# Optimization experiments

Hardware: AMD Instinct MI355X
Metric: run time of the kernel (lower is better)

The kernel has to match this reference:

```python
import jax, jax.numpy as jnp
import numpy as np

N_NODES = 100000
N_EDGES = 3200000


def _norm_weights(edge_index, n):
    # Append self loops (GCNConv gcn_norm adds them back after the module's A - I)
    loops = jnp.arange(n, dtype=edge_index.dtype)
    row = jnp.concatenate([edge_index[0], loops])
    col = jnp.concatenate([edge_index[1], loops])
    ones = jnp.ones(row.shape[0], dtype=jnp.float32)
    deg = jax.ops.segment_sum(ones, row, num_segments=n)
    dinv = jnp.where(deg > 0, jax.lax.rsqrt(deg), 0.0)
    w = dinv[row] * dinv[col]  # symmetric normalization D^-1/2 (A+I) D^-1/2
    return row, col, w


def _spmm(row, col, w, h, n):
    # out[i] = sum_{(i,j) in E} w_ij * h[j]
    return jax.ops.segment_sum(w[:, None] * h[col], row, num_segments=n)


def setup_inputs() -> dict:
    key = jax.random.key(0)
    ks = jax.random.split(key, 4)
    x = jax.random.normal(ks[0], (N_NODES, 512), dtype=jnp.float32)
    W1 = jax.random.normal(ks[1], (512, 16), dtype=jnp.float32) * (1.0 / np.sqrt(512))
    b1 = jnp.zeros((16,), dtype=jnp.float32)
    W2 = jax.random.normal(ks[2], (16, 40), dtype=jnp.float32) * (1.0 / np.sqrt(16))
    b2 = jnp.zeros((40,), dtype=jnp.float32)
    edge_index = jax.random.randint(ks[3], (2, N_EDGES), 0, N_NODES, dtype=jnp.int64)
    return {"x": x, "W1": W1, "b1": b1, "W2": W2, "b2": b2, "edge_index": edge_index}


def reference(x, W1, b1, W2, b2, edge_index):
    n = x.shape[0]
    row, col, w = _norm_weights(edge_index, n)
    # GCNConv layer 1: A_norm @ (x W1) + b1, then relu (dropout is identity in eval)
    h = _spmm(row, col, w, x @ W1, n) + b1
    h = jax.nn.relu(h)
    # GCNConv layer 2 (same adjacency: adj2 is a clone of adj1)
    out = _spmm(row, col, w, h @ W2, n) + b2
    return jax.nn.log_softmax(out, axis=1)
```

## Files before the change

### kernel.cpp

```cpp
#include <hip/hip_runtime.h>
#include <hip/hip_fp16.h>
#include <math.h>

#define F0 512
#define F1 16
#define F2 40
#define CB_SHIFT 8
#define CB_ROWS 256
#define NCB_MAX 512
#define CAPCB 9216
#define EPB 8192
#define COL_BITS 17
#define CMASK ((1 << COL_BITS) - 1)
#define CNT_STRIDE 16

__global__ void k_zero(int* p, int m) {
    int i = blockIdx.x * blockDim.x + threadIdx.x;
    if (i < m) p[i] = 0;
}

__global__ __launch_bounds__(512) void k_fill(const int* __restrict__ row,
                                              const int* __restrict__ col, int E,
                                              int* cnt, int* __restrict__ ebuf,
                                              int NCB) {
    __shared__ int hcnt[NCB_MAX];
    __shared__ int lexcl[NCB_MAX];
    __shared__ int hbase[NCB_MAX];
    __shared__ int part[NCB_MAX];
    __shared__ int sorted[EPB];
    int t = threadIdx.x;
    int e0 = blockIdx.x * EPB;
    int nloc = min(EPB, E - e0);
    if (t < NCB_MAX) hcnt[t] = 0;
    __syncthreads();

    int rr[16], cc[16];
#pragma unroll
    for (int k = 0; k < 4; k++) {
        int base = t * 4 + k * 2048;
        if (base + 3 < nloc) {
            int4 r4 = *(const int4*)(row + e0 + base);
            int4 c4 = *(const int4*)(col + e0 + base);
            rr[k * 4 + 0] = r4.x; rr[k * 4 + 1] = r4.y;
            rr[k * 4 + 2] = r4.z; rr[k * 4 + 3] = r4.w;
            cc[k * 4 + 0] = c4.x; cc[k * 4 + 1] = c4.y;
            cc[k * 4 + 2] = c4.z; cc[k * 4 + 3] = c4.w;
        } else {
#pragma unroll
            for (int q = 0; q < 4; q++) {
                int e = base + q;
                rr[k * 4 + q] = (e < nloc) ? row[e0 + e] : -1;
                cc[k * 4 + q] = (e < nloc) ? col[e0 + e] : 0;
            }
        }
    }
#pragma unroll
    for (int q = 0; q < 16; q++)
        if (rr[q] >= 0) atomicAdd(&hcnt[rr[q] >> CB_SHIFT], 1);
    __syncthreads();
    int myv = hcnt[t];
    part[t] = myv;
    __syncthreads();
    for (int off = 1; off < NCB_MAX; off <<= 1) {
        int a = (t >= off) ? part[t - off] : 0;
        __syncthreads();
        part[t] += a;
        __syncthreads();
    }
    lexcl[t] = part[t] - myv;
    hbase[t] = (myv > 0) ? atomicAdd(&cnt[t * CNT_STRIDE], myv) : 0;
    hcnt[t] = 0;
    __syncthreads();
#pragma unroll
    for (int q = 0; q < 16; q++) {
        int r = rr[q];
        if (r >= 0) {
            int cb = r >> CB_SHIFT;
            int p = lexcl[cb] + atomicAdd(&hcnt[cb], 1);
            sorted[p] = ((r & (CB_ROWS - 1)) << COL_BITS) | cc[q];
        }
    }
    __syncthreads();
    int wv = t >> 6, lane = t & 63;
    for (int cb = wv; cb < NCB; cb += 8) {
        int c = hcnt[cb];
        int ls = lexcl[cb];
        int* dst = ebuf + (size_t)cb * CAPCB + hbase[cb];
        for (int j = lane; j < c; j += 64) dst[j] = sorted[ls + j];
    }
}

__global__ __launch_bounds__(512) void k_scan2(const int* __restrict__ cnt, int NCB,
                                               int* __restrict__ sbbase) {
    __shared__ int part[NCB_MAX];
    int t = threadIdx.x;
    int v = (t < NCB) ? cnt[t * CNT_STRIDE] : 0;
    part[t] = v;
    __syncthreads();
    for (int off = 1; off < NCB_MAX; off <<= 1) {
        int a = (t >= off) ? part[t - off] : 0;
        __syncthreads();
        part[t] += a;
        __syncthreads();
    }
    if (t < NCB) sbbase[t] = part[t] - v;
}

__global__ __launch_bounds__(256) void k_sort(const int* __restrict__ cnt,
                                              const int* __restrict__ sbbase,
                                              const int* __restrict__ ebuf, int n,
                                              int* __restrict__ colsort,
                                              int* __restrict__ deg,
                                              int* __restrict__ rs,
                                              float* __restrict__ dinv) {
    __shared__ int rcnt[CB_ROWS];
    __shared__ int rexcl[CB_ROWS];
    __shared__ int sorted[CAPCB];
    int cb = blockIdx.x;
    int t = threadIdx.x;
    int c = cnt[cb * CNT_STRIDE];
    const int* seg = ebuf + (size_t)cb * CAPCB;
    rcnt[t] = 0;
    __syncthreads();
    for (int base = t * 4; base < c; base += 1024) {
        if (base + 3 < c) {
            int4 v = *(const int4*)(seg + base);
            atomicAdd(&rcnt[v.x >> COL_BITS], 1);
            atomicAdd(&rcnt[v.y >> COL_BITS], 1);
            atomicAdd(&rcnt[v.z >> COL_BITS], 1);
            atomicAdd(&rcnt[v.w >> COL_BITS], 1);
        } else {
            for (int k = base; k < c; k++) atomicAdd(&rcnt[seg[k] >> COL_BITS], 1);
        }
    }
    __syncthreads();
    int myc = rcnt[t];
    rexcl[t] = myc;
    __syncthreads();
    for (int off = 1; off < CB_ROWS; off <<= 1) {
        int a = (t >= off) ? rexcl[t - off] : 0;
        __syncthreads();
        rexcl[t] += a;
        __syncthreads();
    }
    int excl = rexcl[t] - myc;
    int gbase = sbbase[cb];
    int i = (cb << CB_SHIFT) + t;
    if (i < n) {
        deg[i] = myc;
        rs[i] = gbase + excl;
        dinv[i] = rsqrtf((float)(myc + 1));
    }
    rcnt[t] = excl;
    __syncthreads();
    for (int base = t * 4; base < c; base += 1024) {
        if (base + 3 < c) {
            int4 v = *(const int4*)(seg + base);
            int p0 = atomicAdd(&rcnt[v.x >> COL_BITS], 1); sorted[p0] = v.x & CMASK;
            int p1 = atomicAdd(&rcnt[v.y >> COL_BITS], 1); sorted[p1] = v.y & CMASK;
            int p2 = atomicAdd(&rcnt[v.z >> COL_BITS], 1); sorted[p2] = v.z & CMASK;
            int p3 = atomicAdd(&rcnt[v.w >> COL_BITS], 1); sorted[p3] = v.w & CMASK;
        } else {
            for (int k = base; k < c; k++) {
                int v = seg[k];
                int p = atomicAdd(&rcnt[v >> COL_BITS], 1);
                sorted[p] = v & CMASK;
            }
        }
    }
    __syncthreads();
    for (int j = t; j < c; j += 256) colsort[gbase + j] = sorted[j];
}

__global__ __launch_bounds__(256, 2) void k_gemm1(const float* __restrict__ x,
                                                  const float* __restrict__ W1,
                                                  const float* __restrict__ dinv,
                                                  __half* __restrict__ hp, int n,
                                                  int total_waves) {
    int lane = threadIdx.x & 63;
    int wid = blockIdx.x * (blockDim.x >> 6) + (threadIdx.x >> 6);

    float w[8][16];
#pragma unroll
    for (int h = 0; h < 2; h++) {
#pragma unroll
        for (int r = 0; r < 4; r++) {
            int k = h * 256 + 4 * lane + r;
            const float4* p = (const float4*)(W1 + k * 16);
            float4 a = p[0], b = p[1], c = p[2], d = p[3];
            float* wr = w[h * 4 + r];
            wr[0] = a.x; wr[1] = a.y; wr[2] = a.z; wr[3] = a.w;
            wr[4] = b.x; wr[5] = b.y; wr[6] = b.z; wr[7] = b.w;
            wr[8] = c.x; wr[9] = c.y; wr[10] = c.z; wr[11] = c.w;
            wr[12] = d.x; wr[13] = d.y; wr[14] = d.z; wr[15] = d.w;
        }
    }

    for (int i0 = wid * 4; i0 < n; i0 += total_waves * 4) {
        float4 xq[8];
        if (i0 + 3 < n) {
            const float4* xp = (const float4*)(x + (size_t)i0 * F0);
#pragma unroll
            for (int q = 0; q < 8; q++) xq[q] = xp[q * 64 + lane];
        } else {
#pragma unroll
            for (int q = 0; q < 8; q++) {
                int r = q >> 1;
                if (i0 + r < n) {
                    const float4* xp = (const float4*)(x + (size_t)(i0 + r) * F0);
                    xq[q] = xp[(q & 1) * 64 + lane];
                } else {
                    xq[q] = make_float4(0.f, 0.f, 0.f, 0.f);
                }
            }
        }
        bool b0 = (lane & 1) != 0;
        bool b1 = (lane & 2) != 0;
        bool b2 = (lane & 4) != 0;
        bool b3 = (lane & 8) != 0;
#pragma unroll
        for (int r = 0; r < 4; r++) {
            float4 xa = xq[2 * r], xb = xq[2 * r + 1];
            float v16[16];
#pragma unroll
            for (int j = 0; j < 16; j++) {
                v16[j] = xa.x * w[0][j] + xa.y * w[1][j] + xa.z * w[2][j] + xa.w * w[3][j]
                       + xb.x * w[4][j] + xb.y * w[5][j] + xb.z * w[6][j] + xb.w * w[7][j];
            }
            float v8[8];
#pragma unroll
            for (int t2 = 0; t2 < 8; t2++) {
                float a = v16[2 * t2], b = v16[2 * t2 + 1];
                float keep = b0 ? b : a;
                float send = b0 ? a : b;
                v8[t2] = keep + __shfl_xor(send, 1);
            }
            float v4[4];
#pragma unroll
            for (int t2 = 0; t2 < 4; t2++) {
                float a = v8[2 * t2], b = v8[2 * t2 + 1];
                float keep = b1 ? b : a;
                float send = b1 ? a : b;
                v4[t2] = keep + __shfl_xor(send, 2);
            }
            float v2[2];
#pragma unroll
            for (int t2 = 0; t2 < 2; t2++) {
                float a = v4[2 * t2], b = v4[2 * t2 + 1];
                float keep = b2 ? b : a;
                float send = b2 ? a : b;
                v2[t2] = keep + __shfl_xor(send, 4);
            }
            float keep = b3 ? v2[1] : v2[0];
            float send = b3 ? v2[0] : v2[1];
            float v1 = keep + __shfl_xor(send, 8);
            v1 += __shfl_xor(v1, 16);
            v1 += __shfl_xor(v1, 32);
            int i = i0 + r;
            if (lane < 16 && i < n)
                hp[(size_t)i * F1 + lane] = __float2half_rn(dinv[i] * v1);
        }
    }
}

__global__ __launch_bounds__(256) void k_spmm1(const __half* __restrict__ hp,
                                               const int* __restrict__ rs,
                                               const int* __restrict__ deg,
                                               const int* __restrict__ colsort,
                                               const float* __restrict__ dinv,
                                               const float* __restrict__ b1,
                                               __half* __restrict__ s2, int n) {
    int t = threadIdx.x;
    int lane = t & 63;
    int g = lane >> 4;
    int jf = lane & 15;
    int i = blockIdx.x * 4 + (t >> 6);
    if (i >= n) return;
    int s = rs[i], c = deg[i];
    float acc = (g == 0) ? __half2float(hp[(size_t)i * F1 + jf]) : 0.f;
    int e = g;
    for (; e + 12 < c; e += 16) {
        int c0 = colsort[s + e];
        int c1 = colsort[s + e + 4];
        int c2 = colsort[s + e + 8];
        int c3 = colsort[s + e + 12];
        float v0 = __half2float(hp[(size_t)c0 * F1 + jf]);
        float v1 = __half2float(hp[(size_t)c1 * F1 + jf]);
        float v2 = __half2float(hp[(size_t)c2 * F1 + jf]);
        float v3 = __half2float(hp[(size_t)c3 * F1 + jf]);
        acc += (v0 + v1) + (v2 + v3);
    }
    for (; e < c; e += 4)
        acc += __half2float(hp[(size_t)colsort[s + e] * F1 + jf]);
    acc += __shfl_xor(acc, 16);
    acc += __shfl_xor(acc, 32);
    float di = dinv[i];
    float h1 = fmaxf(di * acc + b1[jf], 0.f);
    if (lane < 16) s2[(size_t)i * F1 + jf] = __float2half_rn(di * h1);
}

__global__ __launch_bounds__(256) void k_spmm2(const __half* __restrict__ s2,
                                               const int* __restrict__ rs,
                                               const int* __restrict__ deg,
                                               const int* __restrict__ colsort,
                                               const float* __restrict__ dinv,
                                               const float* __restrict__ W2,
                                               const float* __restrict__ b2,
                                               float* __restrict__ out, int n) {
    __shared__ float sW2[F1 * F2];
    int t = threadIdx.x;
    for (int idx = t; idx < F1 * F2; idx += 256) sW2[idx] = W2[idx];
    __syncthreads();

    int lane = t & 63;
    int g = lane >> 4;
    int jf = lane & 15;
    int i = blockIdx.x * 4 + (t >> 6);
    if (i >= n) return;
    int s = rs[i], c = deg[i];
    float acc = (g == 0) ? __half2float(s2[(size_t)i * F1 + jf]) : 0.f;
    int e = g;
    for (; e + 12 < c; e += 16) {
        int c0 = colsort[s + e];
        int c1 = colsort[s + e + 4];
        int c2 = colsort[s + e + 8];
        int c3 = colsort[s + e + 12];
        float v0 = __half2float(s2[(size_t)c0 * F1 + jf]);
        float v1 = __half2float(s2[(size_t)c1 * F1 + jf]);
        float v2 = __half2float(s2[(size_t)c2 * F1 + jf]);
        float v3 = __half2float(s2[(size_t)c3 * F1 + jf]);
        acc += (v0 + v1) + (v2 + v3);
    }
    for (; e < c; e += 4)
        acc += __half2float(s2[(size_t)colsort[s + e] * F1 + jf]);
    acc += __shfl_xor(acc, 16);
    acc += __shfl_xor(acc, 32);
    float z = dinv[i] * acc;

    bool act = lane < F2;
    int k = act ? lane : 0;
    float o = 0.f;
#pragma unroll
    for (int j = 0; j < F1; j++) {
        float zj = __shfl(z, j);
        o += zj * sW2[j * F2 + k];
    }
    float val = act ? o + b2[k] : -INFINITY;
    float m = val;
#pragma unroll
    for (int off = 1; off < 64; off <<= 1) m = fmaxf(m, __shfl_xor(m, off));
    float ex = act ? __expf(val - m) : 0.f;
    float ssum = ex;
#pragma unroll
    for (int off = 1; off < 64; off <<= 1) ssum += __shfl_xor(ssum, off);
    if (act) out[(size_t)i * F2 + lane] = val - m - __logf(ssum);
}

extern "C" void kernel_launch(void* const* d_in, const int* in_sizes, int n_in,
                              void* d_out, int out_size, void* d_ws, size_t ws_size,
                              hipStream_t stream) {
    const float* x  = (const float*)d_in[0];
    const float* W1 = (const float*)d_in[1];
    const float* b1 = (const float*)d_in[2];
    const float* W2 = (const float*)d_in[3];
    const float* b2 = (const float*)d_in[4];
    const int*   ei = (const int*)d_in[5];

    int n = in_sizes[0] / F0;
    int E = in_sizes[5] / 2;
    const int* row = ei;
    const int* col = ei + E;
    int NCB = (n + CB_ROWS - 1) >> CB_SHIFT;

    int* deg     = (int*)d_ws;
    int* rs      = deg + n;
    float* dinv  = (float*)(rs + n);
    int* cnt     = (int*)(dinv + n);
    int* sbbase  = cnt + NCB_MAX * CNT_STRIDE;
    int* colsort = sbbase + NCB_MAX;
    int* ebuf    = colsort + E;
    __half* hp   = (__half*)ebuf;
    __half* s2   = hp + (size_t)n * F1;

    int nchunks = (E + EPB - 1) / EPB;
    k_zero<<<(NCB * CNT_STRIDE + 255) / 256, 256, 0, stream>>>(cnt, NCB * CNT_STRIDE);
    k_fill<<<nchunks, 512, 0, stream>>>(row, col, E, cnt, ebuf, NCB);
    k_scan2<<<1, NCB_MAX, 0, stream>>>(cnt, NCB, sbbase);
    k_sort<<<NCB, 256, 0, stream>>>(cnt, sbbase, ebuf, n, colsort, deg, rs, dinv);

    int g1_blocks = 2048;
    k_gemm1<<<g1_blocks, 256, 0, stream>>>(x, W1, dinv, hp, n, g1_blocks * 4);
    k_spmm1<<<(n + 3) / 4, 256, 0, stream>>>(hp, rs, deg, colsort, dinv, b1, s2, n);
    k_spmm2<<<(n + 3) / 4, 256, 0, stream>>>(s2, rs, deg, colsort, dinv, W2, b2,
                                             (float*)d_out, n);
}
```

Measured before the change: 478.4 us.

## Map one node per 16 lanes in SpMM kernels instead of one per wavefront

Both SpMM kernels now give each node a 16-lane group rather than a full 64-lane wavefront split into four edge-groups, so a block of 256 threads handles 16 nodes. Each group walks all of its node's edges sequentially with 8-way unrolled gathers, which removes the cross-group shuffle reductions and the idle lanes in the store. The second kernel's dense 16x40 projection and log-softmax are reworked so each lane computes up to three outputs, with reductions done inside the 16-lane group. The cost is longer serial edge loops per lane (about 33 edges per node), which relies on more resident nodes to hide gather latency.

```diff
diff --git a/kernel.cpp b/kernel.cpp
--- a/kernel.cpp
+++ b/kernel.cpp
@@ -271,32 +271,42 @@
                                                const float* __restrict__ b1,
                                                __half* __restrict__ s2, int n) {
     int t = threadIdx.x;
-    int lane = t & 63;
-    int g = lane >> 4;
-    int jf = lane & 15;
-    int i = blockIdx.x * 4 + (t >> 6);
+    int jf = t & 15;
+    int i = blockIdx.x * 16 + (t >> 4);
     if (i >= n) return;
     int s = rs[i], c = deg[i];
-    float acc = (g == 0) ? __half2float(hp[(size_t)i * F1 + jf]) : 0.f;
-    int e = g;
-    for (; e + 12 < c; e += 16) {
-        int c0 = colsort[s + e];
-        int c1 = colsort[s + e + 4];
-        int c2 = colsort[s + e + 8];
-        int c3 = colsort[s + e + 12];
+    const int* cs = colsort + s;
+    float acc = __half2float(hp[(size_t)i * F1 + jf]);
+    int e = 0;
+    for (; e + 7 < c; e += 8) {
+        int c0 = cs[e];     int c1 = cs[e + 1];
+        int c2 = cs[e + 2]; int c3 = cs[e + 3];
+        int c4 = cs[e + 4]; int c5 = cs[e + 5];
+        int c6 = cs[e + 6]; int c7 = cs[e + 7];
+        float v0 = __half2float(hp[(size_t)c0 * F1 + jf]);
+        float v1 = __half2float(hp[(size_t)c1 * F1 + jf]);
+        float v2 = __half2float(hp[(size_t)c2 * F1 + jf]);
+        float v3 = __half2float(hp[(size_t)c3 * F1 + jf]);
+        float v4 = __half2float(hp[(size_t)c4 * F1 + jf]);
+        float v5 = __half2float(hp[(size_t)c5 * F1 + jf]);
+        float v6 = __half2float(hp[(size_t)c6 * F1 + jf]);
+        float v7 = __half2float(hp[(size_t)c7 * F1 + jf]);
+        acc += ((v0 + v1) + (v2 + v3)) + ((v4 + v5) + (v6 + v7));
+    }
+    for (; e + 3 < c; e += 4) {
+        int c0 = cs[e];     int c1 = cs[e + 1];
+        int c2 = cs[e + 2]; int c3 = cs[e + 3];
         float v0 = __half2float(hp[(size_t)c0 * F1 + jf]);
         float v1 = __half2float(hp[(size_t)c1 * F1 + jf]);
         float v2 = __half2float(hp[(size_t)c2 * F1 + jf]);
         float v3 = __half2float(hp[(size_t)c3 * F1 + jf]);
         acc += (v0 + v1) + (v2 + v3);
     }
-    for (; e < c; e += 4)
-        acc += __half2float(hp[(size_t)colsort[s + e] * F1 + jf]);
-    acc += __shfl_xor(acc, 16);
-    acc += __shfl_xor(acc, 32);
+    for (; e < c; e++)
+        acc += __half2float(hp[(size_t)cs[e] * F1 + jf]);
     float di = dinv[i];
     float h1 = fmaxf(di * acc + b1[jf], 0.f);
-    if (lane < 16) s2[(size_t)i * F1 + jf] = __float2half_rn(di * h1);
+    s2[(size_t)i * F1 + jf] = __float2half_rn(di * h1);
 }
 
 __global__ __launch_bounds__(256) void k_spmm2(const __half* __restrict__ s2,
@@ -312,48 +322,65 @@
     for (int idx = t; idx < F1 * F2; idx += 256) sW2[idx] = W2[idx];
     __syncthreads();
 
-    int lane = t & 63;
-    int g = lane >> 4;
-    int jf = lane & 15;
-    int i = blockIdx.x * 4 + (t >> 6);
+    int jf = t & 15;
+    int i = blockIdx.x * 16 + (t >> 4);
     if (i >= n) return;
     int s = rs[i], c = deg[i];
-    float acc = (g == 0) ? __half2float(s2[(size_t)i * F1 + jf]) : 0.f;
-    int e = g;
-    for (; e + 12 < c; e += 16) {
-        int c0 = colsort[s + e];
-        int c1 = colsort[s + e + 4];
-        int c2 = colsort[s + e + 8];
-        int c3 = colsort[s + e + 12];
+    const int* cs = colsort + s;
+    float acc = __half2float(s2[(size_t)i * F1 + jf]);
+    int e = 0;
+    for (; e + 7 < c; e += 8) {
+        int c0 = cs[e];     int c1 = cs[e + 1];
+        int c2 = cs[e + 2]; int c3 = cs[e + 3];
+        int c4 = cs[e + 4]; int c5 = cs[e + 5];
+        int c6 = cs[e + 6]; int c7 = cs[e + 7];
+        float v0 = __half2float(s2[(size_t)c0 * F1 + jf]);
+        float v1 = __half2float(s2[(size_t)c1 * F1 + jf]);
+        float v2 = __half2float(s2[(size_t)c2 * F1 + jf]);
+        float v3 = __half2float(s2[(size_t)c3 * F1 + jf]);
+        float v4 = __half2float(s2[(size_t)c4 * F1 + jf]);
+        float v5 = __half2float(s2[(size_t)c5 * F1 + jf]);
+        float v6 = __half2float(s2[(size_t)c6 * F1 + jf]);
+        float v7 = __half2float(s2[(size_t)c7 * F1 + jf]);
+        acc += ((v0 + v1) + (v2 + v3)) + ((v4 + v5) + (v6 + v7));
+    }
+    for (; e + 3 < c; e += 4) {
+        int c0 = cs[e];     int c1 = cs[e + 1];
+        int c2 = cs[e + 2]; int c3 = cs[e + 3];
         float v0 = __half2float(s2[(size_t)c0 * F1 + jf]);
         float v1 = __half2float(s2[(size_t)c1 * F1 + jf]);
         float v2 = __half2float(s2[(size_t)c2 * F1 + jf]);
         float v3 = __half2float(s2[(size_t)c3 * F1 + jf]);
         acc += (v0 + v1) + (v2 + v3);
     }
-    for (; e < c; e += 4)
-        acc += __half2float(s2[(size_t)colsort[s + e] * F1 + jf]);
-    acc += __shfl_xor(acc, 16);
-    acc += __shfl_xor(acc, 32);
+    for (; e < c; e++)
+        acc += __half2float(s2[(size_t)cs[e] * F1 + jf]);
     float z = dinv[i] * acc;
 
-    bool act = lane < F2;
-    int k = act ? lane : 0;
-    float o = 0.f;
+    int k0 = jf, k1 = jf + 16, k2 = jf + 32;
+    bool has2 = (k2 < F2);
+    float o0 = 0.f, o1 = 0.f, o2 = 0.f;
 #pragma unroll
     for (int j = 0; j < F1; j++) {
-        float zj = __shfl(z, j);
-        o += zj * sW2[j * F2 + k];
-    }
-    float val = act ? o + b2[k] : -INFINITY;
-    float m = val;
-#pragma unroll
-    for (int off = 1; off < 64; off <<= 1) m = fmaxf(m, __shfl_xor(m, off));
-    float ex = act ? __expf(val - m) : 0.f;
-    float ssum = ex;
-#pragma unroll
-    for (int off = 1; off < 64; off <<= 1) ssum += __shfl_xor(ssum, off);
-    if (act) out[(size_t)i * F2 + lane] = val - m - __logf(ssum);
+        float zj = __shfl(z, j, 16);
+        o0 += zj * sW2[j * F2 + k0];
+        o1 += zj * sW2[j * F2 + k1];
+        o2 += zj * sW2[j * F2 + k2 - (has2 ? 0 : 32)];
+    }
+    float v0 = o0 + b2[k0];
+    float v1 = o1 + b2[k1];
+    float v2 = has2 ? (o2 + b2[k2]) : -INFINITY;
+    float m = fmaxf(fmaxf(v0, v1), v2);
+#pragma unroll
+    for (int off = 1; off < 16; off <<= 1) m = fmaxf(m, __shfl_xor(m, off, 16));
+    float ssum = __expf(v0 - m) + __expf(v1 - m) + (has2 ? __expf(v2 - m) : 0.f);
+#pragma unroll
+    for (int off = 1; off < 16; off <<= 1) ssum += __shfl_xor(ssum, off, 16);
+    float lse = m + __logf(ssum);
+    float* orow = out + (size_t)i * F2;
+    orow[k0] = v0 - lse;
+    orow[k1] = v1 - lse;
+    if (has2) orow[k2] = v2 - lse;
 }
 
 extern "C" void kernel_launch(void* const* d_in, const int* in_sizes, int n_in,
@@ -390,7 +417,7 @@
 
     int g1_blocks = 2048;
     k_gemm1<<<g1_blocks, 256, 0, stream>>>(x, W1, dinv, hp, n, g1_blocks * 4);
-    k_spmm1<<<(n + 3) / 4, 256, 0, stream>>>(hp, rs, deg, colsort, dinv, b1, s2, n);
-    k_spmm2<<<(n + 3) / 4, 256, 0, stream>>>(s2, rs, deg, colsort, dinv, W2, b2,
-                                             (float*)d_out, n);
-}
+    k_spmm1<<<(n + 15) / 16, 256, 0, stream>>>(hp, rs, deg, colsort, dinv, b1, s2, n);
+    k_spmm2<<<(n + 15) / 16, 256, 0, stream>>>(s2, rs, deg, colsort, dinv, W2, b2,
+                                               (float*)d_out, n);
+}
```

Result: faster. 429.7 us (-10.2%).

## Remap SpMM kernels to few lanes per node with vectorized half loads

Applied to the files above, without the earlier changes.

Both SpMM kernels now give each node a small group of threads instead of a full wavefront. In spmm1 that is 4 threads, each loading 4 halves as a float2. In spmm2 it is 8 threads, each loading a half2. Each thread walks every edge itself with an 8-way unrolled gather, so no cross-group shuffle reduction is needed. The spmm2 epilogue does the W2 projection and log-softmax within the 8-lane group, each lane producing 5 outputs. This is meant to cut idle lanes and shuffle overhead on nodes with about 33 edges, at the cost of more loads in flight per thread and less coalescing per gather.

```diff
diff --git a/kernel.cpp b/kernel.cpp
--- a/kernel.cpp
+++ b/kernel.cpp
@@ -271,32 +271,54 @@
                                                const float* __restrict__ b1,
                                                __half* __restrict__ s2, int n) {
     int t = threadIdx.x;
-    int lane = t & 63;
-    int g = lane >> 4;
-    int jf = lane & 15;
-    int i = blockIdx.x * 4 + (t >> 6);
+    int jq = t & 3;
+    int i = blockIdx.x * 64 + (t >> 2);
     if (i >= n) return;
     int s = rs[i], c = deg[i];
-    float acc = (g == 0) ? __half2float(hp[(size_t)i * F1 + jf]) : 0.f;
-    int e = g;
-    for (; e + 12 < c; e += 16) {
-        int c0 = colsort[s + e];
-        int c1 = colsort[s + e + 4];
-        int c2 = colsort[s + e + 8];
-        int c3 = colsort[s + e + 12];
-        float v0 = __half2float(hp[(size_t)c0 * F1 + jf]);
-        float v1 = __half2float(hp[(size_t)c1 * F1 + jf]);
-        float v2 = __half2float(hp[(size_t)c2 * F1 + jf]);
-        float v3 = __half2float(hp[(size_t)c3 * F1 + jf]);
-        acc += (v0 + v1) + (v2 + v3);
-    }
-    for (; e < c; e += 4)
-        acc += __half2float(hp[(size_t)colsort[s + e] * F1 + jf]);
-    acc += __shfl_xor(acc, 16);
-    acc += __shfl_xor(acc, 32);
+    const int* cs = colsort + s;
+
+    float4 acc;
+    {
+        float2 r = *(const float2*)(hp + (size_t)i * F1 + 4 * jq);
+        __half2 h01 = *(__half2*)&r.x;
+        __half2 h23 = *(__half2*)&r.y;
+        float2 f01 = __half22float2(h01), f23 = __half22float2(h23);
+        acc = make_float4(f01.x, f01.y, f23.x, f23.y);
+    }
+    int e = 0;
+    for (; e + 7 < c; e += 8) {
+        int cc[8];
+#pragma unroll
+        for (int q = 0; q < 8; q++) cc[q] = cs[e + q];
+        float2 rr[8];
+#pragma unroll
+        for (int q = 0; q < 8; q++)
+            rr[q] = *(const float2*)(hp + (size_t)cc[q] * F1 + 4 * jq);
+#pragma unroll
+        for (int q = 0; q < 8; q++) {
+            __half2 h01 = *(__half2*)&rr[q].x;
+            __half2 h23 = *(__half2*)&rr[q].y;
+            float2 f01 = __half22float2(h01), f23 = __half22float2(h23);
+            acc.x += f01.x; acc.y += f01.y; acc.z += f23.x; acc.w += f23.y;
+        }
+    }
+    for (; e < c; e++) {
+        float2 r = *(const float2*)(hp + (size_t)cs[e] * F1 + 4 * jq);
+        __half2 h01 = *(__half2*)&r.x;
+        __half2 h23 = *(__half2*)&r.y;
+        float2 f01 = __half22float2(h01), f23 = __half22float2(h23);
+        acc.x += f01.x; acc.y += f01.y; acc.z += f23.x; acc.w += f23.y;
+    }
     float di = dinv[i];
-    float h1 = fmaxf(di * acc + b1[jf], 0.f);
-    if (lane < 16) s2[(size_t)i * F1 + jf] = __float2half_rn(di * h1);
+    float4 bb = *(const float4*)(b1 + 4 * jq);
+    float h0 = fmaxf(di * acc.x + bb.x, 0.f);
+    float h1 = fmaxf(di * acc.y + bb.y, 0.f);
+    float h2 = fmaxf(di * acc.z + bb.z, 0.f);
+    float h3 = fmaxf(di * acc.w + bb.w, 0.f);
+    float2 ov;
+    *(__half2*)&ov.x = __floats2half2_rn(di * h0, di * h1);
+    *(__half2*)&ov.y = __floats2half2_rn(di * h2, di * h3);
+    *(float2*)(s2 + (size_t)i * F1 + 4 * jq) = ov;
 }
 
 __global__ __launch_bounds__(256) void k_spmm2(const __half* __restrict__ s2,
@@ -312,48 +334,63 @@
     for (int idx = t; idx < F1 * F2; idx += 256) sW2[idx] = W2[idx];
     __syncthreads();
 
-    int lane = t & 63;
-    int g = lane >> 4;
-    int jf = lane & 15;
-    int i = blockIdx.x * 4 + (t >> 6);
+    int jh = t & 7;
+    int i = blockIdx.x * 32 + (t >> 3);
     if (i >= n) return;
     int s = rs[i], c = deg[i];
-    float acc = (g == 0) ? __half2float(s2[(size_t)i * F1 + jf]) : 0.f;
-    int e = g;
-    for (; e + 12 < c; e += 16) {
-        int c0 = colsort[s + e];
-        int c1 = colsort[s + e + 4];
-        int c2 = colsort[s + e + 8];
-        int c3 = colsort[s + e + 12];
-        float v0 = __half2float(s2[(size_t)c0 * F1 + jf]);
-        float v1 = __half2float(s2[(size_t)c1 * F1 + jf]);
-        float v2 = __half2float(s2[(size_t)c2 * F1 + jf]);
-        float v3 = __half2float(s2[(size_t)c3 * F1 + jf]);
-        acc += (v0 + v1) + (v2 + v3);
-    }
-    for (; e < c; e += 4)
-        acc += __half2float(s2[(size_t)colsort[s + e] * F1 + jf]);
-    acc += __shfl_xor(acc, 16);
-    acc += __shfl_xor(acc, 32);
-    float z = dinv[i] * acc;
-
-    bool act = lane < F2;
-    int k = act ? lane : 0;
-    float o = 0.f;
-#pragma unroll
-    for (int j = 0; j < F1; j++) {
-        float zj = __shfl(z, j);
-        o += zj * sW2[j * F2 + k];
-    }
-    float val = act ? o + b2[k] : -INFINITY;
-    float m = val;
-#pragma unroll
-    for (int off = 1; off < 64; off <<= 1) m = fmaxf(m, __shfl_xor(m, off));
-    float ex = act ? __expf(val - m) : 0.f;
-    float ssum = ex;
-#pragma unroll
-    for (int off = 1; off < 64; off <<= 1) ssum += __shfl_xor(ssum, off);
-    if (act) out[(size_t)i * F2 + lane] = val - m - __logf(ssum);
+    const int* cs = colsort + s;
+    float2 acc = __half22float2(*(const __half2*)(s2 + (size_t)i * F1 + 2 * jh));
+    int e = 0;
+    for (; e + 7 < c; e += 8) {
+        int cc[8];
+#pragma unroll
+        for (int q = 0; q < 8; q++) cc[q] = cs[e + q];
+        __half2 hh[8];
+#pragma unroll
+        for (int q = 0; q < 8; q++)
+            hh[q] = *(const __half2*)(s2 + (size_t)cc[q] * F1 + 2 * jh);
+#pragma unroll
+        for (int q = 0; q < 8; q++) {
+            float2 f = __half22float2(hh[q]);
+            acc.x += f.x; acc.y += f.y;
+        }
+    }
+    for (; e < c; e++) {
+        float2 f = __half22float2(*(const __half2*)(s2 + (size_t)cs[e] * F1 + 2 * jh));
+        acc.x += f.x; acc.y += f.y;
+    }
+    float di = dinv[i];
+    float zx0 = di * acc.x, zy0 = di * acc.y;
+
+    float o[5] = {0.f, 0.f, 0.f, 0.f, 0.f};
+#pragma unroll
+    for (int sl = 0; sl < 8; sl++) {
+        float zx = __shfl(zx0, sl, 8);
+        float zy = __shfl(zy0, sl, 8);
+#pragma unroll
+        for (int q = 0; q < 5; q++) {
+            int k = jh + 8 * q;
+            o[q] += zx * sW2[(2 * sl) * F2 + k] + zy * sW2[(2 * sl + 1) * F2 + k];
+        }
+    }
+    float v[5];
+    float m = -INFINITY;
+#pragma unroll
+    for (int q = 0; q < 5; q++) {
+        v[q] = o[q] + b2[jh + 8 * q];
+        m = fmaxf(m, v[q]);
+    }
+#pragma unroll
+    for (int off = 1; off < 8; off <<= 1) m = fmaxf(m, __shfl_xor(m, off, 8));
+    float ssum = 0.f;
+#pragma unroll
+    for (int q = 0; q < 5; q++) ssum += __expf(v[q] - m);
+#pragma unroll
+    for (int off = 1; off < 8; off <<= 1) ssum += __shfl_xor(ssum, off, 8);
+    float lse = m + __logf(ssum);
+    float* orow = out + (size_t)i * F2;
+#pragma unroll
+    for (int q = 0; q < 5; q++) orow[jh + 8 * q] = v[q] - lse;
 }
 
 extern "C" void kernel_launch(void* const* d_in, const int* in_sizes, int n_in,
@@ -390,7 +427,7 @@
 
     int g1_blocks = 2048;
     k_gemm1<<<g1_blocks, 256, 0, stream>>>(x, W1, dinv, hp, n, g1_blocks * 4);
-    k_spmm1<<<(n + 3) / 4, 256, 0, stream>>>(hp, rs, deg, colsort, dinv, b1, s2, n);
-    k_spmm2<<<(n + 3) / 4, 256, 0, stream>>>(s2, rs, deg, colsort, dinv, W2, b2,
-                                             (float*)d_out, n);
-}
+    k_spmm1<<<(n + 63) / 64, 256, 0, stream>>>(hp, rs, deg, colsort, dinv, b1, s2, n);
+    k_spmm2<<<(n + 31) / 32, 256, 0, stream>>>(s2, rs, deg, colsort, dinv, W2, b2,
+                                               (float*)d_out, n);
+}
```

New measurement: 424.0 us, median of 2. 1.13x faster.
